# Optimization experiments

Measured on AMD Instinct MI355X. Metric: run time of the kernel, lower is better.

Reference implementation:

```python
import math
import jax, jax.numpy as jnp
import numpy as np

B, T, C = 2, 2048, 1024
H, D = 16, 64
QC, KC = 128, 256
SCALE = 1.0 / math.sqrt(D)


def _int4_linear(x, w_int8, scale, bias):
    # W = dequant(int8) * per-output-channel scale; y = x @ W.T + bias
    w = w_int8.astype(jnp.float32) * scale[:, None]
    return x @ w.T + bias


def _attention_recompute(q, k, v):
    # q,k,v: (B,H,T,D). Williams-style 2D tiling with streaming (online) softmax, causal.
    nq, nk = T // QC, T // KC
    qt = q.reshape(B, H, nq, QC, D).transpose(2, 0, 1, 3, 4)  # (nq,B,H,QC,D)
    kt = k.reshape(B, H, nk, KC, D).transpose(2, 0, 1, 3, 4)  # (nk,B,H,KC,D)
    vt = v.reshape(B, H, nk, KC, D).transpose(2, 0, 1, 3, 4)
    q_idx = jnp.arange(T).reshape(nq, QC)
    k_idx = jnp.arange(T).reshape(nk, KC)

    def per_qchunk(q_tile, q_pos):
        def step(carry, inp):
            m, l, o = carry
            k_c, v_c, k_pos = inp
            s = jnp.einsum('bhqd,bhkd->bhqk', q_tile, k_c) * SCALE
            mask = k_pos[None, None, None, :] <= q_pos[None, None, :, None]
            s = jnp.where(mask, s, -jnp.inf)
            s_max = jnp.max(s, axis=-1, keepdims=True)
            m_new = jnp.maximum(m, s_max)
            alpha = jnp.exp(m - m_new)
            p = jnp.exp(s - m_new)
            o = o * alpha + jnp.einsum('bhqk,bhkd->bhqd', p, v_c)
            l = l * alpha + jnp.sum(p, axis=-1, keepdims=True)
            return (m_new, l, o), None

        m0 = jnp.full((B, H, QC, 1), -jnp.inf, dtype=q_tile.dtype)
        l0 = jnp.zeros((B, H, QC, 1), dtype=q_tile.dtype)
        o0 = jnp.zeros_like(q_tile)
        (m, l, o), _ = jax.lax.scan(step, (m0, l0, o0), (kt, vt, k_idx))
        return o / (l + 1e-8)

    out = jax.vmap(per_qchunk)(qt, q_idx)  # (nq,B,H,QC,D)
    return out.transpose(1, 2, 0, 3, 4).reshape(B, H, T, D)


def _forward(x, wq, sq, bq, wk, sk, bk, wv, sv, bv, wo, so, bo):
    q = _int4_linear(x, wq, sq, bq).reshape(B, T, H, D).transpose(0, 2, 1, 3)
    k = _int4_linear(x, wk, sk, bk).reshape(B, T, H, D).transpose(0, 2, 1, 3)
    v = _int4_linear(x, wv, sv, bv).reshape(B, T, H, D).transpose(0, 2, 1, 3)
    attn = _attention_recompute(q, k, v)
    y = attn.transpose(0, 2, 1, 3).reshape(B, T, C)
    return _int4_linear(y, wo, so, bo)


def setup_inputs() -> dict:
    key = jax.random.key(0)
    ks = jax.random.split(key, 5)
    x = jax.random.normal(ks[0], (B, T, C), dtype=jnp.float32)

    def w(k):
        return jax.random.randint(k, (C, C), -8, 8, dtype=jnp.int8)

    s = 0.005 * jnp.ones((C,), jnp.float32)  # trainable per-channel scale (init shrunk for sane activations)
    b = jnp.zeros((C,), jnp.float32)
    return {
        'x': x,
        'wq': w(ks[1]), 'sq': s, 'bq': b,
        'wk': w(ks[2]), 'sk': s, 'bk': b,
        'wv': w(ks[3]), 'sv': s, 'bv': b,
        'wo': w(ks[4]), 'so': s, 'bo': b,
    }


def reference(x, wq, sq, bq, wk, sk, bk, wv, sv, bv, wo, so, bo):
    return _forward(x, wq, sq, bq, wk, sk, bk, wv, sv, bv, wo, so, bo)
```

## Files before the change

### kernel.cpp

```cpp
#include <hip/hip_runtime.h>
#include <hip/hip_bf16.h>
#include <stdint.h>

#define BB 2
#define TT 2048
#define CC 1024
#define HH 16
#define DD 64
#define MM (BB*TT)

typedef __bf16 bf16x8 __attribute__((ext_vector_type(8)));
typedef float  f32x4  __attribute__((ext_vector_type(4)));
typedef float  f32x16 __attribute__((ext_vector_type(16)));
typedef unsigned short u16;
typedef unsigned int   u32;

__device__ __forceinline__ u16 f2bf(float f) {
  u32 u = __float_as_uint(f);
  return (u16)((u + 0x7fffu + ((u >> 16) & 1u)) >> 16);
}

__device__ __forceinline__ u32 cvt_pk_bf16(float a, float b) {
  u32 r;
  asm("v_cvt_pk_bf16_f32 %0, %1, %2" : "=v"(r) : "v"(a), "v"(b));
  return r;
}

__device__ __forceinline__ void gload_lds16(const u16* g, u16* l) {
  auto gp = (const u32 __attribute__((address_space(1)))*)(uintptr_t)g;
  auto lp = (u32 __attribute__((address_space(3)))*)(u32)(uintptr_t)l;
  __builtin_amdgcn_global_load_lds(gp, lp, 16, 0, 0);
}

__global__ __launch_bounds__(256)
void k_sentinel(float* __restrict__ out, int n) {
  int i = blockIdx.x * 256 + threadIdx.x;
  if (i < n) out[i] = 9999.0f;
}

__global__ __launch_bounds__(256)
void k_convert(const float* __restrict__ x,
               const int* __restrict__ w0, const int* __restrict__ w1,
               const int* __restrict__ w2, const int* __restrict__ w3,
               u16* __restrict__ xb, u16* __restrict__ wb) {
  const int idx = blockIdx.x * 256 + threadIdx.x;
  const int NX = MM * CC / 4;
  if (idx < NX) {
    float4 v = ((const float4*)x)[idx];
    u32 lo = (u32)f2bf(v.x) | ((u32)f2bf(v.y) << 16);
    u32 hi = (u32)f2bf(v.z) | ((u32)f2bf(v.w) << 16);
    ((uint2*)xb)[idx] = make_uint2(lo, hi);
  } else {
    int u = idx - NX;
    int mat = u >> 18;
    int j = u & 262143;
    const int* ws = (mat == 0) ? w0 : (mat == 1) ? w1 : (mat == 2) ? w2 : w3;
    int4 v = ((const int4*)ws)[j];
    u32 lo = (u32)f2bf((float)v.x) | ((u32)f2bf((float)v.y) << 16);
    u32 hi = (u32)f2bf((float)v.z) | ((u32)f2bf((float)v.w) << 16);
    ((uint2*)wb)[(mat << 18) + j] = make_uint2(lo, hi);
  }
}

__device__ __forceinline__ void gemm_core(const u16* __restrict__ Ag,
                                          const u16* __restrict__ Wg,
                                          int brow, int bcol,
                                          u16* As, u16* Bs, f32x4 acc[4][4]) {
  const int tid  = threadIdx.x;
  const int w    = tid >> 6;
  const int lane = tid & 63;
  const int q = lane & 15, g = lane >> 4;
  const int wm = w >> 1, wn = w & 1;

  for (int kt = 0; kt < CC / 32; ++kt) {
    #pragma unroll
    for (int i = 0; i < 2; ++i) {
      int Lg  = i * 256 + tid;
      int row = Lg >> 2, gc = Lg & 3;
      gload_lds16(Ag + (brow + row) * CC + kt * 32 + gc * 8, As + (i * 256 + w * 64) * 8);
      gload_lds16(Wg + (bcol + row) * CC + kt * 32 + gc * 8, Bs + (i * 256 + w * 64) * 8);
    }
    __syncthreads();
    bf16x8 af[4], bff[4];
    #pragma unroll
    for (int a = 0; a < 4; ++a) af[a]  = *(const bf16x8*)&As[(wm * 64 + a * 16 + q) * 32 + g * 8];
    #pragma unroll
    for (int b = 0; b < 4; ++b) bff[b] = *(const bf16x8*)&Bs[(wn * 64 + b * 16 + q) * 32 + g * 8];
    #pragma unroll
    for (int a = 0; a < 4; ++a) {
      #pragma unroll
      for (int b = 0; b < 4; ++b) {
        acc[a][b] = __builtin_amdgcn_mfma_f32_16x16x32_bf16(af[a], bff[b], acc[a][b], 0, 0, 0);
      }
    }
    __syncthreads();
  }
}

__global__ __launch_bounds__(256)
void k_gemm_qkv(const u16* __restrict__ xb, const u16* __restrict__ wb,
                const float* __restrict__ sq, const float* __restrict__ bq,
                const float* __restrict__ sk, const float* __restrict__ bk,
                const float* __restrict__ sv, const float* __restrict__ bv,
                u16* __restrict__ Qo, u16* __restrict__ Ko, u16* __restrict__ Vt) {
  __shared__ u16 As[128 * 32];
  __shared__ u16 Bs[128 * 32];
  const int bid  = blockIdx.x;
  const int brow = (bid & 31) * 128;
  const int ncol = (bid >> 5) * 128;
  const int mat  = ncol >> 10;
  const int bcol = ncol & 1023;
  const u16* W = wb + (mat << 20);

  f32x4 acc[4][4];
  #pragma unroll
  for (int a = 0; a < 4; ++a)
    #pragma unroll
    for (int b = 0; b < 4; ++b) { f32x4 z = {0.f, 0.f, 0.f, 0.f}; acc[a][b] = z; }

  gemm_core(xb, W, brow, bcol, As, Bs, acc);

  const int tid = threadIdx.x;
  const int w = tid >> 6, lane = tid & 63;
  const int q = lane & 15, g = lane >> 4;
  const int wm = w >> 1, wn = w & 1;
  const float* sarr = (mat == 0) ? sq : (mat == 1) ? sk : sv;
  const float* barr = (mat == 0) ? bq : (mat == 1) ? bk : bv;

  #pragma unroll
  for (int bt = 0; bt < 4; ++bt) {
    const int c = bcol + wn * 64 + bt * 16 + q;
    const float sc = sarr[c];
    const float bi = barr[c];
    const int h = c >> 6, d = c & 63;
    #pragma unroll
    for (int a = 0; a < 4; ++a) {
      #pragma unroll
      for (int r = 0; r < 4; ++r) {
        const int m = brow + wm * 64 + a * 16 + 4 * g + r;
        const int b_ = m >> 11, t = m & 2047;
        const u16 val = f2bf(acc[a][bt][r] * sc + bi);
        if (mat == 0)      Qo[(((size_t)(b_ * HH + h) * TT) + t) * DD + d] = val;
        else if (mat == 1) Ko[(((size_t)(b_ * HH + h) * TT) + t) * DD + d] = val;
        else               Vt[((size_t)(b_ * HH + h) * DD + d) * TT + t] = val;
      }
    }
  }
}

__global__ __launch_bounds__(256, 2)
void k_attn(const u16* __restrict__ Q, const u16* __restrict__ K,
            const u16* __restrict__ Vt, u16* __restrict__ Y) {
  __shared__ u16 kbuf[2][2][64 * 64];
  __shared__ u16 vbuf[2][2][64 * 64];
  const int tid = threadIdx.x;
  const int w = tid >> 6, lane = tid & 63;
  const int q = lane & 31, hi = lane >> 5;
  const int r = w >> 1, u_ = w & 1;
  const int bid = blockIdx.x;
  const int bh = bid & 31;
  const int j  = (bid >> 5) & 7;
  const int qt = bid >> 8;
  const int v  = (qt == 0) ? (31 - j) : (qt == 1) ? (16 + j)
               : (qt == 2) ? (15 - j) : j;
  const int qw = v * 64 + 32 * r;
  const int qg = qw + q;
  const u16* Qh = Q  + (size_t)bh * TT * DD;
  const u16* Kh = K  + (size_t)bh * TT * DD;
  const u16* Vh = Vt + (size_t)bh * DD * TT;
  const int b_ = bh >> 4, h = bh & 15;
  constexpr float SE = 0.125f * 1.44269504088896340736f;

  bf16x8 qf[4];
  #pragma unroll
  for (int c = 0; c < 4; ++c)
    qf[c] = *(const bf16x8*)&Qh[(qw + q) * DD + 16 * c + 8 * hi];

  f32x16 oacc[2];
  oacc[0] = f32x16{}; oacc[1] = f32x16{};
  float m_run = -1.0e30f;
  float l_vec[8];
  #pragma unroll
  for (int u2 = 0; u2 < 8; ++u2) l_vec[u2] = 0.f;

  const int nkb = v + 1;
  const int P = (nkb + 1) >> 1;

  #define STAGE(BUFI, PH)                                                           \
    {                                                                               \
      int kbA = min(128 * (PH), TT - 64);                                           \
      int kbB = min(128 * (PH) + 64, TT - 64);                                      \
      _Pragma("unroll")                                                             \
      for (int jj = 0; jj < 2; ++jj) {                                              \
        int kbase_j = jj ? kbB : kbA;                                               \
        _Pragma("unroll")                                                           \
        for (int r2 = 0; r2 < 2; ++r2) {                                            \
          int g = r2 * 256 + tid;                                                   \
          int row = g >> 3, cB = (g & 7) << 4;                                      \
          int scB = cB ^ ((row & 7) << 4);                                          \
          gload_lds16(Kh + (size_t)(kbase_j + row) * DD + (scB >> 1),               \
                      &kbuf[BUFI][jj][(r2 * 256 + w * 64) * 8]);                    \
        }                                                                           \
        _Pragma("unroll")                                                           \
        for (int r2 = 0; r2 < 2; ++r2) {                                            \
          int g = r2 * 256 + tid;                                                   \
          int row = g >> 3, cB = (g & 7) << 4;                                      \
          int scB = cB ^ ((row & 7) << 4);                                          \
          gload_lds16(Vh + (size_t)row * TT + kbase_j + (scB >> 1),                 \
                      &vbuf[BUFI][jj][(r2 * 256 + w * 64) * 8]);                    \
        }                                                                           \
      }                                                                             \
    }

  STAGE(0, 0);
  for (int i = 0; i < P; ++i) {
    asm volatile("s_waitcnt vmcnt(0)" ::: "memory");
    __builtin_amdgcn_s_barrier();
    __builtin_amdgcn_sched_barrier(0);
    if (i + 1 < P) STAGE((i + 1) & 1, i + 1);

    const int kb2 = 2 * i + u_;
    if (kb2 < nkb) {
      const int kbase = kb2 * 64;
      const u16* kl = kbuf[i & 1][u_];
      const u16* vl = vbuf[i & 1][u_];

      bf16x8 kf[2][4];
      #pragma unroll
      for (int s = 0; s < 2; ++s)
        #pragma unroll
        for (int c = 0; c < 4; ++c) {
          const int row = 32 * s + q, cB = 32 * c + 16 * hi;
          kf[s][c] = *(const bf16x8*)&kl[(row * 128 + (cB ^ ((row & 7) << 4))) >> 1];
        }
      f32x16 sacc[2];
      sacc[0] = f32x16{}; sacc[1] = f32x16{};
      __builtin_amdgcn_s_setprio(1);
      #pragma unroll
      for (int c = 0; c < 4; ++c) {
        sacc[0] = __builtin_amdgcn_mfma_f32_32x32x16_bf16(kf[0][c], qf[c], sacc[0], 0, 0, 0);
        sacc[1] = __builtin_amdgcn_mfma_f32_32x32x16_bf16(kf[1][c], qf[c], sacc[1], 0, 0, 0);
      }
      __builtin_amdgcn_s_setprio(0);

      bf16x8 vf[2][2][2];
      #pragma unroll
      for (int dt = 0; dt < 2; ++dt)
        #pragma unroll
        for (int s = 0; s < 2; ++s)
          #pragma unroll
          for (int c2 = 0; c2 < 2; ++c2) {
            const int row = dt * 32 + q, cB = 64 * s + 32 * c2 + 16 * hi;
            vf[dt][s][c2] = *(const bf16x8*)&vl[(row * 128 + (cB ^ ((row & 7) << 4))) >> 1];
          }

      float sr[32];
      #pragma unroll
      for (int s = 0; s < 2; ++s)
        #pragma unroll
        for (int rr = 0; rr < 16; ++rr) sr[s * 16 + rr] = sacc[s][rr];
      if (kbase + 63 > qw) {
        #pragma unroll
        for (int s = 0; s < 2; ++s)
          #pragma unroll
          for (int rr = 0; rr < 16; ++rr)
            if (kbase + 32 * s + (rr & 3) + 8 * (rr >> 2) + 4 * hi > qg)
              sr[s * 16 + rr] = -__builtin_inff();
      }
      float mx[16];
      #pragma unroll
      for (int u2 = 0; u2 < 16; ++u2) mx[u2] = fmaxf(sr[u2], sr[u2 + 16]);
      #pragma unroll
      for (int st = 8; st > 0; st >>= 1)
        #pragma unroll
        for (int u2 = 0; u2 < st; ++u2) mx[u2] = fmaxf(mx[u2], mx[u2 + st]);
      const float pmax = fmaxf(mx[0], __shfl_xor(mx[0], 32)) * SE;
      const bool keep = __all(pmax <= m_run + 8.0f);
      const float m_new = keep ? m_run : fmaxf(m_run, pmax);
      const float nm = -m_new;
      float p[32];
      #pragma unroll
      for (int u2 = 0; u2 < 32; ++u2)
        p[u2] = __builtin_amdgcn_exp2f(fmaf(sr[u2], SE, nm));
      if (!keep) {
        const float alpha = __builtin_amdgcn_exp2f(m_run - m_new);
        m_run = m_new;
        oacc[0] *= alpha;
        oacc[1] *= alpha;
        #pragma unroll
        for (int u2 = 0; u2 < 8; ++u2) l_vec[u2] *= alpha;
      }
      float t16[16];
      #pragma unroll
      for (int u2 = 0; u2 < 16; ++u2) t16[u2] = p[u2] + p[u2 + 16];
      #pragma unroll
      for (int u2 = 0; u2 < 8; ++u2) l_vec[u2] += t16[u2] + t16[u2 + 8];

      u32 Aw[8], Bw[8];
      #pragma unroll
      for (int n = 0; n < 8; ++n) {
        const int base = ((n >> 2) * 16) + ((n & 3) << 2);
        Aw[n] = cvt_pk_bf16(p[base + 0], p[base + 1]);
        Bw[n] = cvt_pk_bf16(p[base + 2], p[base + 3]);
      }
      bf16x8 pf[2][2];
      #pragma unroll
      for (int s = 0; s < 2; ++s)
        #pragma unroll
        for (int c2 = 0; c2 < 2; ++c2) {
          const int n0 = 4 * s + 2 * c2;
          u32 x0 = Aw[n0], x2 = Aw[n0 + 1];
          asm volatile("v_permlane32_swap_b32 %0, %1" : "+v"(x0), "+v"(x2));
          u32 x1 = Bw[n0], x3 = Bw[n0 + 1];
          asm volatile("v_permlane32_swap_b32 %0, %1" : "+v"(x1), "+v"(x3));
          union { u32 uw[4]; bf16x8 vv; } U;
          U.uw[0] = x0; U.uw[1] = x1; U.uw[2] = x2; U.uw[3] = x3;
          pf[s][c2] = U.vv;
        }

      __builtin_amdgcn_s_setprio(1);
      #pragma unroll
      for (int s = 0; s < 2; ++s)
        #pragma unroll
        for (int c2 = 0; c2 < 2; ++c2) {
          oacc[0] = __builtin_amdgcn_mfma_f32_32x32x16_bf16(vf[0][s][c2], pf[s][c2], oacc[0], 0, 0, 0);
          oacc[1] = __builtin_amdgcn_mfma_f32_32x32x16_bf16(vf[1][s][c2], pf[s][c2], oacc[1], 0, 0, 0);
        }
      __builtin_amdgcn_s_setprio(0);
    }
  }
  #undef STAGE

  __syncthreads();
  float l_run = ((l_vec[0] + l_vec[1]) + (l_vec[2] + l_vec[3]))
              + ((l_vec[4] + l_vec[5]) + (l_vec[6] + l_vec[7]));
  float* ms = ((float*)kbuf) + (r * 64 + lane) * 37;
  if (u_ == 1) {
    #pragma unroll
    for (int dt = 0; dt < 2; ++dt)
      #pragma unroll
      for (int e = 0; e < 16; ++e) ms[dt * 16 + e] = oacc[dt][e];
    ms[32] = m_run;
    ms[33] = l_run;
  }
  __syncthreads();
  if (u_ == 0) {
    const float m1 = ms[32], l1 = ms[33];
    const float mt = fmaxf(m_run, m1);
    const float s0 = __builtin_amdgcn_exp2f(m_run - mt);
    const float s1 = __builtin_amdgcn_exp2f(m1 - mt);
    float lt = l_run * s0 + l1 * s1;
    lt += __shfl_xor(lt, 32);
    const float inv = 1.f / (lt + 1e-8f);
    #pragma unroll
    for (int dt = 0; dt < 2; ++dt)
      #pragma unroll
      for (int n = 0; n < 4; ++n) {
        const float o0 = (oacc[dt][4 * n + 0] * s0 + ms[dt * 16 + 4 * n + 0] * s1) * inv;
        const float o1 = (oacc[dt][4 * n + 1] * s0 + ms[dt * 16 + 4 * n + 1] * s1) * inv;
        const float o2 = (oacc[dt][4 * n + 2] * s0 + ms[dt * 16 + 4 * n + 2] * s1) * inv;
        const float o3 = (oacc[dt][4 * n + 3] * s0 + ms[dt * 16 + 4 * n + 3] * s1) * inv;
        u32 lo  = cvt_pk_bf16(o0, o1);
        u32 hi2 = cvt_pk_bf16(o2, o3);
        *(uint2*)&Y[(size_t)(b_ * TT + qg) * CC + h * 64 + 32 * dt + 8 * n + 4 * hi]
          = make_uint2(lo, hi2);
      }
  }
}

__global__ __launch_bounds__(256)
void k_gemm_o(const u16* __restrict__ Yb, const u16* __restrict__ Wo,
              const float* __restrict__ so, const float* __restrict__ bo,
              float* __restrict__ out) {
  __shared__ u16 As[128 * 32];
  __shared__ u16 Bs[64 * 32];
  const int bid = blockIdx.x;
  const int brow = (bid & 31) * 128;
  const int bcol = (bid >> 5) * 64;
  const int tid  = threadIdx.x;
  const int w    = tid >> 6;
  const int lane = tid & 63;
  const int q = lane & 15, g = lane >> 4;
  const int wm = w >> 1, wn = w & 1;

  f32x4 acc[4][2];
  #pragma unroll
  for (int a = 0; a < 4; ++a)
    #pragma unroll
    for (int b = 0; b < 2; ++b) { f32x4 z = {0.f, 0.f, 0.f, 0.f}; acc[a][b] = z; }

  for (int kt = 0; kt < CC / 32; ++kt) {
    #pragma unroll
    for (int i = 0; i < 2; ++i) {
      int Lg  = i * 256 + tid;
      int row = Lg >> 2, gc = Lg & 3;
      gload_lds16(Yb + (size_t)(brow + row) * CC + kt * 32 + gc * 8, As + (i * 256 + w * 64) * 8);
    }
    {
      int row = tid >> 2, gc = tid & 3;
      gload_lds16(Wo + (size_t)(bcol + row) * CC + kt * 32 + gc * 8, Bs + (w * 64) * 8);
    }
    __syncthreads();
    bf16x8 af[4], bff[2];
    #pragma unroll
    for (int a = 0; a < 4; ++a) af[a]  = *(const bf16x8*)&As[(wm * 64 + a * 16 + q) * 32 + g * 8];
    #pragma unroll
    for (int b = 0; b < 2; ++b) bff[b] = *(const bf16x8*)&Bs[(wn * 32 + b * 16 + q) * 32 + g * 8];
    #pragma unroll
    for (int a = 0; a < 4; ++a) {
      #pragma unroll
      for (int b = 0; b < 2; ++b) {
        acc[a][b] = __builtin_amdgcn_mfma_f32_16x16x32_bf16(af[a], bff[b], acc[a][b], 0, 0, 0);
      }
    }
    __syncthreads();
  }

  #pragma unroll
  for (int bt = 0; bt < 2; ++bt) {
    const int c = bcol + wn * 32 + bt * 16 + q;
    const float sc = so[c], bi = bo[c];
    #pragma unroll
    for (int a = 0; a < 4; ++a) {
      const int mbase = brow + wm * 64 + a * 16 + 4 * g;
      #pragma unroll
      for (int r = 0; r < 4; ++r) {
        out[(size_t)(mbase + r) * CC + c] = acc[a][bt][r] * sc + bi;
      }
    }
  }
}

extern "C" void kernel_launch(void* const* d_in, const int* in_sizes, int n_in,
                              void* d_out, int out_size, void* d_ws, size_t ws_size,
                              hipStream_t stream) {
  const float* x  = (const float*)d_in[0];
  const int*   wq = (const int*)d_in[1];
  const float* sq = (const float*)d_in[2];
  const float* bq = (const float*)d_in[3];
  const int*   wk = (const int*)d_in[4];
  const float* sk = (const float*)d_in[5];
  const float* bk = (const float*)d_in[6];
  const int*   wv = (const int*)d_in[7];
  const float* sv = (const float*)d_in[8];
  const float* bv = (const float*)d_in[9];
  const int*   wo = (const int*)d_in[10];
  const float* so = (const float*)d_in[11];
  const float* bo = (const float*)d_in[12];

  const size_t NEED = (40u << 20);
  if (ws_size < NEED) {
    k_sentinel<<<dim3((out_size + 255) / 256), dim3(256), 0, stream>>>((float*)d_out, out_size);
    return;
  }

  char* ws = (char*)d_ws;
  u16* xb = (u16*)(ws);
  u16* wb = (u16*)(ws + (8u  << 20));
  u16* Qb = (u16*)(ws + (16u << 20));
  u16* Kb = (u16*)(ws + (24u << 20));
  u16* Vt = (u16*)(ws + (32u << 20));
  u16* Yb = xb;

  k_convert <<<dim3(8192), dim3(256), 0, stream>>>(x, wq, wk, wv, wo, xb, wb);
  k_gemm_qkv<<<dim3(768),  dim3(256), 0, stream>>>(xb, wb, sq, bq, sk, bk, sv, bv, Qb, Kb, Vt);
  k_attn    <<<dim3(1024), dim3(256), 0, stream>>>(Qb, Kb, Vt, Yb);
  k_gemm_o  <<<dim3(512),  dim3(256), 0, stream>>>(Yb, wb + (3u << 20), so, bo, (float*)d_out);
}
```

Measured before the change: 105.1 us.

## Triple-buffer QKV GEMM LDS loads with async prefetch two stages ahead

Replaces the single-buffered QKV projection GEMM loop with a three-stage LDS ring. Global-to-LDS loads are issued two K-tiles ahead, with a partial vmcnt wait and one barrier per iteration instead of two, so memory latency can overlap MFMA work. It also raises wave priority around the MFMA block. This triples LDS use per block, which may lower occupancy, and correctness depends on the hand-counted vmcnt values.

```diff
diff --git a/kernel.cpp b/kernel.cpp
--- a/kernel.cpp
+++ b/kernel.cpp
@@ -62,71 +62,75 @@
   }
 }
 
-__device__ __forceinline__ void gemm_core(const u16* __restrict__ Ag,
-                                          const u16* __restrict__ Wg,
-                                          int brow, int bcol,
-                                          u16* As, u16* Bs, f32x4 acc[4][4]) {
-  const int tid  = threadIdx.x;
-  const int w    = tid >> 6;
-  const int lane = tid & 63;
-  const int q = lane & 15, g = lane >> 4;
-  const int wm = w >> 1, wn = w & 1;
-
-  for (int kt = 0; kt < CC / 32; ++kt) {
-    #pragma unroll
-    for (int i = 0; i < 2; ++i) {
-      int Lg  = i * 256 + tid;
-      int row = Lg >> 2, gc = Lg & 3;
-      gload_lds16(Ag + (brow + row) * CC + kt * 32 + gc * 8, As + (i * 256 + w * 64) * 8);
-      gload_lds16(Wg + (bcol + row) * CC + kt * 32 + gc * 8, Bs + (i * 256 + w * 64) * 8);
-    }
-    __syncthreads();
-    bf16x8 af[4], bff[4];
-    #pragma unroll
-    for (int a = 0; a < 4; ++a) af[a]  = *(const bf16x8*)&As[(wm * 64 + a * 16 + q) * 32 + g * 8];
-    #pragma unroll
-    for (int b = 0; b < 4; ++b) bff[b] = *(const bf16x8*)&Bs[(wn * 64 + b * 16 + q) * 32 + g * 8];
-    #pragma unroll
-    for (int a = 0; a < 4; ++a) {
-      #pragma unroll
-      for (int b = 0; b < 4; ++b) {
-        acc[a][b] = __builtin_amdgcn_mfma_f32_16x16x32_bf16(af[a], bff[b], acc[a][b], 0, 0, 0);
-      }
-    }
-    __syncthreads();
-  }
-}
-
 __global__ __launch_bounds__(256)
 void k_gemm_qkv(const u16* __restrict__ xb, const u16* __restrict__ wb,
                 const float* __restrict__ sq, const float* __restrict__ bq,
                 const float* __restrict__ sk, const float* __restrict__ bk,
                 const float* __restrict__ sv, const float* __restrict__ bv,
                 u16* __restrict__ Qo, u16* __restrict__ Ko, u16* __restrict__ Vt) {
-  __shared__ u16 As[128 * 32];
-  __shared__ u16 Bs[128 * 32];
+  __shared__ u16 As[3][4096];
+  __shared__ u16 Bs[3][4096];
   const int bid  = blockIdx.x;
   const int brow = (bid & 31) * 128;
   const int ncol = (bid >> 5) * 128;
   const int mat  = ncol >> 10;
   const int bcol = ncol & 1023;
   const u16* W = wb + (mat << 20);
-
-  f32x4 acc[4][4];
-  #pragma unroll
-  for (int a = 0; a < 4; ++a)
-    #pragma unroll
-    for (int b = 0; b < 4; ++b) { f32x4 z = {0.f, 0.f, 0.f, 0.f}; acc[a][b] = z; }
-
-  gemm_core(xb, W, brow, bcol, As, Bs, acc);
-
-  const int tid = threadIdx.x;
-  const int w = tid >> 6, lane = tid & 63;
+  const int tid  = threadIdx.x;
+  const int w    = tid >> 6;
+  const int lane = tid & 63;
   const int q = lane & 15, g = lane >> 4;
   const int wm = w >> 1, wn = w & 1;
+
+  f32x4 acc[4][4];
+  #pragma unroll
+  for (int a = 0; a < 4; ++a)
+    #pragma unroll
+    for (int b = 0; b < 4; ++b) { f32x4 z = {0.f, 0.f, 0.f, 0.f}; acc[a][b] = z; }
+
+  #define QSTAGE(BUF, KT)                                                        \
+    {                                                                            \
+      _Pragma("unroll")                                                          \
+      for (int i2 = 0; i2 < 2; ++i2) {                                           \
+        int Lg = i2 * 256 + tid;                                                 \
+        int row = Lg >> 2, gc = Lg & 3;                                          \
+        gload_lds16(xb + (size_t)(brow + row) * CC + (KT) * 32 + gc * 8,         \
+                    &As[BUF][(i2 * 256 + w * 64) * 8]);                          \
+        gload_lds16(W  + (size_t)(bcol + row) * CC + (KT) * 32 + gc * 8,         \
+                    &Bs[BUF][(i2 * 256 + w * 64) * 8]);                          \
+      }                                                                          \
+    }
+
+  QSTAGE(0, 0);
+  QSTAGE(1, 1);
+  for (int kt = 0; kt < CC / 32; ++kt) {
+    if (kt < CC / 32 - 1) asm volatile("s_waitcnt vmcnt(4)" ::: "memory");
+    else                  asm volatile("s_waitcnt vmcnt(0)" ::: "memory");
+    __builtin_amdgcn_s_barrier();
+    __builtin_amdgcn_sched_barrier(0);
+    if (kt + 2 < CC / 32) QSTAGE((kt + 2) % 3, kt + 2);
+
+    const u16* Asb = As[kt % 3];
+    const u16* Bsb = Bs[kt % 3];
+    bf16x8 af[4], bff[4];
+    #pragma unroll
+    for (int a = 0; a < 4; ++a) af[a]  = *(const bf16x8*)&Asb[(wm * 64 + a * 16 + q) * 32 + g * 8];
+    #pragma unroll
+    for (int b = 0; b < 4; ++b) bff[b] = *(const bf16x8*)&Bsb[(wn * 64 + b * 16 + q) * 32 + g * 8];
+    __builtin_amdgcn_s_setprio(1);
+    #pragma unroll
+    for (int a = 0; a < 4; ++a) {
+      #pragma unroll
+      for (int b = 0; b < 4; ++b) {
+        acc[a][b] = __builtin_amdgcn_mfma_f32_16x16x32_bf16(af[a], bff[b], acc[a][b], 0, 0, 0);
+      }
+    }
+    __builtin_amdgcn_s_setprio(0);
+  }
+  #undef QSTAGE
+
   const float* sarr = (mat == 0) ? sq : (mat == 1) ? sk : sv;
   const float* barr = (mat == 0) ? bq : (mat == 1) ? bk : bv;
-
   #pragma unroll
   for (int bt = 0; bt < 4; ++bt) {
     const int c = bcol + wn * 64 + bt * 16 + q;
```

New measurement: 107.0 us. Within noise of the previous version (+1.8%).
